# Performance work log

Measured on AMD Instinct MI355X. Metric: run time of the kernel, lower is better.

## Reference

```python
import jax, jax.numpy as jnp
import numpy as np

MAX_DISTANCE = 50.0
NUM_BINS = 50
FEATURE_DIM = 64
B, K = 2048, 1024


def setup_inputs() -> dict:
    key = jax.random.key(0)
    k1, k2, k3, k4, k5, k6 = jax.random.split(key, 6)
    goal_positions = jax.random.normal(k1, (B, K, 2), dtype=jnp.float32) * 20.0
    ego_state = jax.random.normal(k2, (B, 4), dtype=jnp.float32)
    in_dim = NUM_BINS + 6  # 56
    s1 = 1.0 / np.sqrt(in_dim)
    s2 = 1.0 / np.sqrt(FEATURE_DIM)
    W1 = jax.random.uniform(k3, (in_dim, FEATURE_DIM), jnp.float32, -s1, s1)
    b1 = jax.random.uniform(k4, (FEATURE_DIM,), jnp.float32, -s1, s1)
    W2 = jax.random.uniform(k5, (FEATURE_DIM, 1), jnp.float32, -s2, s2)
    b2 = jax.random.uniform(k6, (1,), jnp.float32, -s2, s2)
    return {"goal_positions": goal_positions, "ego_state": ego_state,
            "W1": W1, "b1": b1, "W2": W2, "b2": b2}


def _histogram(goal_positions):
    # distances: (B, K); bin_idx = min(int(d / max_d * num_bins), num_bins - 1)
    d = jnp.linalg.norm(goal_positions, axis=-1)
    idx = jnp.floor(d / MAX_DISTANCE * NUM_BINS).astype(jnp.int32)
    idx = jnp.clip(idx, 0, NUM_BINS - 1)
    return jax.nn.one_hot(idx, NUM_BINS, dtype=goal_positions.dtype)  # (B, K, num_bins)


def reference(goal_positions, ego_state, W1, b1, W2, b2):
    hist = _histogram(goal_positions)                              # (B, K, nb)
    ego = jnp.broadcast_to(ego_state[:, None, :],
                           (goal_positions.shape[0], goal_positions.shape[1], 4))
    feats = jnp.concatenate([hist, goal_positions, ego], axis=-1)  # (B, K, nb+6)
    h = jax.nn.relu(jnp.einsum('bkf,fd->bkd', feats, W1) + b1)     # (B, K, feature_dim)
    scores = (jnp.einsum('bkd,do->bko', h, W2) + b2)[..., 0]       # (B, K)
    return scores
```

## Files before the change

kernel.cpp:

```cpp
#include <hip/hip_runtime.h>

#define NBIN 50
#define DIM  64
#define KPT  4
#define TPB  256

__global__ __launch_bounds__(TPB, 8) void scorer_kernel(
    const float* __restrict__ goal,
    const float* __restrict__ ego,
    const float* __restrict__ W1,
    const float* __restrict__ b1,
    const float* __restrict__ W2,
    const float* __restrict__ b2,
    float* __restrict__ out,
    int K)
{
    __shared__ float4 comb[16 * NBIN];
    __shared__ float  e_lds[DIM];

    const int b   = blockIdx.x;
    const int tid = threadIdx.x;

    const float4 eg = ((const float4*)ego)[b];
    if (tid < DIM) {
        float v = b1[tid]
                + eg.x * W1[52 * DIM + tid]
                + eg.y * W1[53 * DIM + tid]
                + eg.z * W1[54 * DIM + tid]
                + eg.w * W1[55 * DIM + tid];
        e_lds[tid] = v;
    }
    __syncthreads();

    for (int i = tid; i < NBIN * DIM; i += TPB) {
        int bin = i >> 6;
        int d   = i & 63;
        float v = W1[i] + e_lds[d];
        ((float*)comb)[(((d >> 2) * NBIN) + bin) * 4 + (d & 3)] = v;
    }
    __syncthreads();

    const float2* gp   = (const float2*)goal + (size_t)b * K;
    const float4* w50v = (const float4*)(W1 + 50 * DIM);
    const float4* w51v = (const float4*)(W1 + 51 * DIM);
    const float4* w2v  = (const float4*)W2;
    const float  bias2 = b2[0];

    float2 p[KPT];
    int    idx[KPT];
    float  acc[KPT];

#pragma unroll
    for (int j = 0; j < KPT; ++j) {
        int k = j * TPB + tid;
        p[j] = gp[k];
        float r2 = __fadd_rn(__fmul_rn(p[j].x, p[j].x), __fmul_rn(p[j].y, p[j].y));
        float r  = __fsqrt_rn(r2);
        float fv = floorf(__fmul_rn(__fdiv_rn(r, 50.0f), 50.0f));
        int ix = (int)fv;
        ix = ix < 0 ? 0 : (ix > NBIN - 1 ? NBIN - 1 : ix);
        idx[j] = ix;
        acc[j] = 0.0f;
    }

#pragma unroll
    for (int d4 = 0; d4 < 16; ++d4) {
        const float4 a  = w50v[d4];
        const float4 bb = w51v[d4];
        const float4 c  = w2v[d4];
#pragma unroll
        for (int j = 0; j < KPT; ++j) {
            const float4 g = comb[d4 * NBIN + idx[j]];
            float x = p[j].x, y = p[j].y;
            float t0 = fmaf(x, a.x, fmaf(y, bb.x, g.x));
            float t1 = fmaf(x, a.y, fmaf(y, bb.y, g.y));
            float t2 = fmaf(x, a.z, fmaf(y, bb.z, g.z));
            float t3 = fmaf(x, a.w, fmaf(y, bb.w, g.w));
            acc[j] = fmaf(c.x, fmaxf(t0, 0.0f), acc[j]);
            acc[j] = fmaf(c.y, fmaxf(t1, 0.0f), acc[j]);
            acc[j] = fmaf(c.z, fmaxf(t2, 0.0f), acc[j]);
            acc[j] = fmaf(c.w, fmaxf(t3, 0.0f), acc[j]);
        }
    }

    float* po = out + (size_t)b * K;
#pragma unroll
    for (int j = 0; j < KPT; ++j) {
        po[j * TPB + tid] = acc[j] + bias2;
    }
}

extern "C" void kernel_launch(void* const* d_in, const int* in_sizes, int n_in,
                              void* d_out, int out_size, void* d_ws, size_t ws_size,
                              hipStream_t stream) {
    const float* goal = (const float*)d_in[0];
    const float* ego  = (const float*)d_in[1];
    const float* W1   = (const float*)d_in[2];
    const float* b1   = (const float*)d_in[3];
    const float* W2   = (const float*)d_in[4];
    const float* b2   = (const float*)d_in[5];
    float* out = (float*)d_out;

    int B = in_sizes[1] / 4;
    int K = in_sizes[0] / (2 * B);

    scorer_kernel<<<dim3(B), dim3(TPB), 0, stream>>>(goal, ego, W1, b1, W2, b2, out, K);
}
```

Baseline: 21.94 us.

## Store combined bin table as bf16 and vectorize goal loads/stores per thread

Result: slower. 25.06 us (+14.2%).

```diff
diff --git a/kernel.cpp b/kernel.cpp
--- a/kernel.cpp
+++ b/kernel.cpp
@@ -2,10 +2,17 @@
 
 #define NBIN 50
 #define DIM  64
+#define TPB  256
 #define KPT  4
-#define TPB  256
 
-__global__ __launch_bounds__(TPB, 8) void scorer_kernel(
+__device__ __forceinline__ float u32_as_f32(unsigned int u) {
+    union { unsigned int u; float f; } c; c.u = u; return c.f;
+}
+__device__ __forceinline__ unsigned int f32_bits(float f) {
+    union { float f; unsigned int u; } c; c.f = f; return c.u;
+}
+
+__global__ __launch_bounds__(TPB, 4) void scorer_kernel(
     const float* __restrict__ goal,
     const float* __restrict__ ego,
     const float* __restrict__ W1,
@@ -15,20 +22,19 @@
     float* __restrict__ out,
     int K)
 {
-    __shared__ float4 comb[16 * NBIN];
-    __shared__ float  e_lds[DIM];
+    __shared__ alignas(16) unsigned short comb[8 * NBIN * 8];
+    __shared__ float e_lds[DIM];
 
     const int b   = blockIdx.x;
     const int tid = threadIdx.x;
 
     const float4 eg = ((const float4*)ego)[b];
     if (tid < DIM) {
-        float v = b1[tid]
-                + eg.x * W1[52 * DIM + tid]
-                + eg.y * W1[53 * DIM + tid]
-                + eg.z * W1[54 * DIM + tid]
-                + eg.w * W1[55 * DIM + tid];
-        e_lds[tid] = v;
+        e_lds[tid] = b1[tid]
+                   + eg.x * W1[52 * DIM + tid]
+                   + eg.y * W1[53 * DIM + tid]
+                   + eg.z * W1[54 * DIM + tid]
+                   + eg.w * W1[55 * DIM + tid];
     }
     __syncthreads();
 
@@ -36,58 +42,79 @@
         int bin = i >> 6;
         int d   = i & 63;
         float v = W1[i] + e_lds[d];
-        ((float*)comb)[(((d >> 2) * NBIN) + bin) * 4 + (d & 3)] = v;
+        unsigned int u = f32_bits(v);
+        unsigned int r = (u + 0x7fffu + ((u >> 16) & 1u)) >> 16;
+        comb[((d >> 3) * NBIN + bin) * 8 + (d & 7)] = (unsigned short)r;
     }
     __syncthreads();
 
-    const float2* gp   = (const float2*)goal + (size_t)b * K;
-    const float4* w50v = (const float4*)(W1 + 50 * DIM);
-    const float4* w51v = (const float4*)(W1 + 51 * DIM);
-    const float4* w2v  = (const float4*)W2;
-    const float  bias2 = b2[0];
+    const float4* gp4 = (const float4*)goal + (size_t)b * (K / 2);
+    const float4  ga  = gp4[tid * 2];
+    const float4  gb  = gp4[tid * 2 + 1];
 
     float2 p[KPT];
     int    idx[KPT];
     float  acc[KPT];
+    p[0] = make_float2(ga.x, ga.y);
+    p[1] = make_float2(ga.z, ga.w);
+    p[2] = make_float2(gb.x, gb.y);
+    p[3] = make_float2(gb.z, gb.w);
 
 #pragma unroll
     for (int j = 0; j < KPT; ++j) {
-        int k = j * TPB + tid;
-        p[j] = gp[k];
         float r2 = __fadd_rn(__fmul_rn(p[j].x, p[j].x), __fmul_rn(p[j].y, p[j].y));
-        float r  = __fsqrt_rn(r2);
-        float fv = floorf(__fmul_rn(__fdiv_rn(r, 50.0f), 50.0f));
+        float fv = floorf(__fmul_rn(__fdiv_rn(__fsqrt_rn(r2), 50.0f), 50.0f));
         int ix = (int)fv;
-        ix = ix < 0 ? 0 : (ix > NBIN - 1 ? NBIN - 1 : ix);
-        idx[j] = ix;
+        idx[j] = ix < 0 ? 0 : (ix > NBIN - 1 ? NBIN - 1 : ix);
         acc[j] = 0.0f;
     }
 
+    const float4* w50v  = (const float4*)(W1 + 50 * DIM);
+    const float4* w51v  = (const float4*)(W1 + 51 * DIM);
+    const float4* w2v   = (const float4*)W2;
+    const uint4*  combv = (const uint4*)comb;
+    const float   bias2 = b2[0];
+
 #pragma unroll
-    for (int d4 = 0; d4 < 16; ++d4) {
-        const float4 a  = w50v[d4];
-        const float4 bb = w51v[d4];
-        const float4 c  = w2v[d4];
+    for (int d8 = 0; d8 < 8; ++d8) {
+        const float4 a0 = w50v[d8 * 2];
+        const float4 a1 = w50v[d8 * 2 + 1];
+        const float4 q0 = w51v[d8 * 2];
+        const float4 q1 = w51v[d8 * 2 + 1];
+        const float4 c0 = w2v[d8 * 2];
+        const float4 c1 = w2v[d8 * 2 + 1];
 #pragma unroll
         for (int j = 0; j < KPT; ++j) {
-            const float4 g = comb[d4 * NBIN + idx[j]];
-            float x = p[j].x, y = p[j].y;
-            float t0 = fmaf(x, a.x, fmaf(y, bb.x, g.x));
-            float t1 = fmaf(x, a.y, fmaf(y, bb.y, g.y));
-            float t2 = fmaf(x, a.z, fmaf(y, bb.z, g.z));
-            float t3 = fmaf(x, a.w, fmaf(y, bb.w, g.w));
-            acc[j] = fmaf(c.x, fmaxf(t0, 0.0f), acc[j]);
-            acc[j] = fmaf(c.y, fmaxf(t1, 0.0f), acc[j]);
-            acc[j] = fmaf(c.z, fmaxf(t2, 0.0f), acc[j]);
-            acc[j] = fmaf(c.w, fmaxf(t3, 0.0f), acc[j]);
+            const uint4 g = combv[d8 * NBIN + idx[j]];
+            const float x = p[j].x, y = p[j].y;
+            float s = acc[j];
+            float h0 = u32_as_f32(g.x << 16), h1 = u32_as_f32(g.x & 0xffff0000u);
+            float h2 = u32_as_f32(g.y << 16), h3 = u32_as_f32(g.y & 0xffff0000u);
+            float h4 = u32_as_f32(g.z << 16), h5 = u32_as_f32(g.z & 0xffff0000u);
+            float h6 = u32_as_f32(g.w << 16), h7 = u32_as_f32(g.w & 0xffff0000u);
+            float t0 = fmaf(x, a0.x, fmaf(y, q0.x, h0));
+            float t1 = fmaf(x, a0.y, fmaf(y, q0.y, h1));
+            float t2 = fmaf(x, a0.z, fmaf(y, q0.z, h2));
+            float t3 = fmaf(x, a0.w, fmaf(y, q0.w, h3));
+            float t4 = fmaf(x, a1.x, fmaf(y, q1.x, h4));
+            float t5 = fmaf(x, a1.y, fmaf(y, q1.y, h5));
+            float t6 = fmaf(x, a1.z, fmaf(y, q1.z, h6));
+            float t7 = fmaf(x, a1.w, fmaf(y, q1.w, h7));
+            s = fmaf(c0.x, fmaxf(t0, 0.0f), s);
+            s = fmaf(c0.y, fmaxf(t1, 0.0f), s);
+            s = fmaf(c0.z, fmaxf(t2, 0.0f), s);
+            s = fmaf(c0.w, fmaxf(t3, 0.0f), s);
+            s = fmaf(c1.x, fmaxf(t4, 0.0f), s);
+            s = fmaf(c1.y, fmaxf(t5, 0.0f), s);
+            s = fmaf(c1.z, fmaxf(t6, 0.0f), s);
+            s = fmaf(c1.w, fmaxf(t7, 0.0f), s);
+            acc[j] = s;
         }
     }
 
-    float* po = out + (size_t)b * K;
-#pragma unroll
-    for (int j = 0; j < KPT; ++j) {
-        po[j * TPB + tid] = acc[j] + bias2;
-    }
+    float4 res = make_float4(acc[0] + bias2, acc[1] + bias2,
+                             acc[2] + bias2, acc[3] + bias2);
+    ((float4*)out)[(size_t)b * (K / 4) + tid] = res;
 }
 
 extern "C" void kernel_launch(void* const* d_in, const int* in_sizes, int n_in,
```

## Counting-sort points by bin in LDS to avoid bank conflicts in combined-table lookups

Applied to the files above, without the earlier changes.

Result: slower. 23.71 us (+8.0%).

```diff
diff --git a/kernel.cpp b/kernel.cpp
--- a/kernel.cpp
+++ b/kernel.cpp
@@ -2,80 +2,118 @@
 
 #define NBIN 50
 #define DIM  64
+#define TPB  256
 #define KPT  4
-#define TPB  256
+#define KMAX (TPB * KPT)
 
-__global__ __launch_bounds__(TPB, 8) void scorer_kernel(
+__global__ __launch_bounds__(TPB, 5) void scorer_kernel(
     const float* __restrict__ goal,
     const float* __restrict__ ego,
     const float* __restrict__ W1,
     const float* __restrict__ b1,
     const float* __restrict__ W2,
     const float* __restrict__ b2,
-    float* __restrict__ out,
-    int K)
+    float* __restrict__ out)
 {
     __shared__ float4 comb[16 * NBIN];
     __shared__ float  e_lds[DIM];
+    __shared__ float2 sxy[KMAX];
+    __shared__ unsigned short smeta[KMAX];
+    __shared__ int    cnt[NBIN];
+    __shared__ int    pfx[NBIN];
+    __shared__ float  sout[KMAX];
 
     const int b   = blockIdx.x;
     const int tid = threadIdx.x;
 
-    const float4 eg = ((const float4*)ego)[b];
+    const float4* gp4 = (const float4*)goal + (size_t)b * (KMAX / 2);
+    const float4  ga  = gp4[tid * 2];
+    const float4  gb  = gp4[tid * 2 + 1];
+    const float4  eg  = ((const float4*)ego)[b];
+
     if (tid < DIM) {
-        float v = b1[tid]
-                + eg.x * W1[52 * DIM + tid]
-                + eg.y * W1[53 * DIM + tid]
-                + eg.z * W1[54 * DIM + tid]
-                + eg.w * W1[55 * DIM + tid];
-        e_lds[tid] = v;
+        e_lds[tid] = b1[tid]
+                   + eg.x * W1[52 * DIM + tid]
+                   + eg.y * W1[53 * DIM + tid]
+                   + eg.z * W1[54 * DIM + tid]
+                   + eg.w * W1[55 * DIM + tid];
+    }
+    if (tid < NBIN) cnt[tid] = 0;
+    __syncthreads();
+
+    float2 p[KPT];
+    p[0] = make_float2(ga.x, ga.y);
+    p[1] = make_float2(ga.z, ga.w);
+    p[2] = make_float2(gb.x, gb.y);
+    p[3] = make_float2(gb.z, gb.w);
+
+    int bin[KPT], rnk[KPT];
+#pragma unroll
+    for (int j = 0; j < KPT; ++j) {
+        float r2 = __fadd_rn(__fmul_rn(p[j].x, p[j].x), __fmul_rn(p[j].y, p[j].y));
+        float fv = floorf(__fmul_rn(__fdiv_rn(__fsqrt_rn(r2), 50.0f), 50.0f));
+        int ix = (int)fv;
+        bin[j] = ix < 0 ? 0 : (ix > NBIN - 1 ? NBIN - 1 : ix);
+        rnk[j] = atomicAdd(&cnt[bin[j]], 1);
+    }
+    for (int i = tid; i < NBIN * DIM; i += TPB) {
+        int bn = i >> 6;
+        int d  = i & 63;
+        ((float*)comb)[(((d >> 2) * NBIN) + bn) * 4 + (d & 3)] = W1[i] + e_lds[d];
     }
     __syncthreads();
 
-    for (int i = tid; i < NBIN * DIM; i += TPB) {
-        int bin = i >> 6;
-        int d   = i & 63;
-        float v = W1[i] + e_lds[d];
-        ((float*)comb)[(((d >> 2) * NBIN) + bin) * 4 + (d & 3)] = v;
+    if (tid < 64) {
+        int v = (tid < NBIN) ? cnt[tid] : 0;
+        int incl = v;
+#pragma unroll
+        for (int d = 1; d < 64; d <<= 1) {
+            int up = __shfl_up(incl, d, 64);
+            if (tid >= d) incl += up;
+        }
+        if (tid < NBIN) pfx[tid] = incl - v;
     }
     __syncthreads();
 
-    const float2* gp   = (const float2*)goal + (size_t)b * K;
+#pragma unroll
+    for (int j = 0; j < KPT; ++j) {
+        int pos = pfx[bin[j]] + rnk[j];
+        sxy[pos]   = p[j];
+        smeta[pos] = (unsigned short)((tid * KPT + j) | (bin[j] << 10));
+    }
+    __syncthreads();
+
     const float4* w50v = (const float4*)(W1 + 50 * DIM);
     const float4* w51v = (const float4*)(W1 + 51 * DIM);
     const float4* w2v  = (const float4*)W2;
     const float  bias2 = b2[0];
 
-    float2 p[KPT];
-    int    idx[KPT];
+    float2 q[KPT];
+    int    sb[KPT], sk[KPT];
     float  acc[KPT];
-
 #pragma unroll
     for (int j = 0; j < KPT; ++j) {
-        int k = j * TPB + tid;
-        p[j] = gp[k];
-        float r2 = __fadd_rn(__fmul_rn(p[j].x, p[j].x), __fmul_rn(p[j].y, p[j].y));
-        float r  = __fsqrt_rn(r2);
-        float fv = floorf(__fmul_rn(__fdiv_rn(r, 50.0f), 50.0f));
-        int ix = (int)fv;
-        ix = ix < 0 ? 0 : (ix > NBIN - 1 ? NBIN - 1 : ix);
-        idx[j] = ix;
+        int s = j * TPB + tid;
+        q[j]  = sxy[s];
+        int m = smeta[s];
+        sk[j] = m & (KMAX - 1);
+        sb[j] = m >> 10;
         acc[j] = 0.0f;
     }
 
 #pragma unroll
     for (int d4 = 0; d4 < 16; ++d4) {
-        const float4 a  = w50v[d4];
-        const float4 bb = w51v[d4];
-        const float4 c  = w2v[d4];
+        const float4 a = w50v[d4];
+        const float4 u = w51v[d4];
+        const float4 c = w2v[d4];
 #pragma unroll
         for (int j = 0; j < KPT; ++j) {
-            const float4 g = comb[d4 * NBIN + idx[j]];
-            float x = p[j].x, y = p[j].y;
-            float t0 = fmaf(x, a.x, fmaf(y, bb.x, g.x));
-            float t1 = fmaf(x, a.y, fmaf(y, bb.y, g.y));
-            float t2 = fmaf(x, a.z, fmaf(y, bb.z, g.z));
-            float t3 = fmaf(x, a.w, fmaf(y, bb.w, g.w));
+            const float4 g = comb[d4 * NBIN + sb[j]];
+            const float x = q[j].x, y = q[j].y;
+            float t0 = fmaf(x, a.x, fmaf(y, u.x, g.x));
+            float t1 = fmaf(x, a.y, fmaf(y, u.y, g.y));
+            float t2 = fmaf(x, a.z, fmaf(y, u.z, g.z));
+            float t3 = fmaf(x, a.w, fmaf(y, u.w, g.w));
             acc[j] = fmaf(c.x, fmaxf(t0, 0.0f), acc[j]);
             acc[j] = fmaf(c.y, fmaxf(t1, 0.0f), acc[j]);
             acc[j] = fmaf(c.z, fmaxf(t2, 0.0f), acc[j]);
@@ -83,11 +121,13 @@
         }
     }
 
-    float* po = out + (size_t)b * K;
 #pragma unroll
-    for (int j = 0; j < KPT; ++j) {
-        po[j * TPB + tid] = acc[j] + bias2;
-    }
+    for (int j = 0; j < KPT; ++j) sout[sk[j]] = acc[j] + bias2;
+    __syncthreads();
+
+    float4 res = make_float4(sout[tid * 4], sout[tid * 4 + 1],
+                             sout[tid * 4 + 2], sout[tid * 4 + 3]);
+    ((float4*)out)[(size_t)b * (KMAX / 4) + tid] = res;
 }
 
 extern "C" void kernel_launch(void* const* d_in, const int* in_sizes, int n_in,
@@ -102,7 +142,5 @@
     float* out = (float*)d_out;
 
     int B = in_sizes[1] / 4;
-    int K = in_sizes[0] / (2 * B);
-
-    scorer_kernel<<<dim3(B), dim3(TPB), 0, stream>>>(goal, ego, W1, b1, W2, b2, out, K);
+    scorer_kernel<<<dim3(B), dim3(TPB), 0, stream>>>(goal, ego, W1, b1, W2, b2, out);
 }
```

## Use packed FP32 FMA, 512 threads, two points per thread, fused setup

Applied to the files above, without the earlier changes.

Measured after the change: 23.58 us. +7.5%, slower.

```diff
diff --git a/kernel.cpp b/kernel.cpp
--- a/kernel.cpp
+++ b/kernel.cpp
@@ -2,8 +2,19 @@
 
 #define NBIN 50
 #define DIM  64
-#define KPT  4
-#define TPB  256
+#define TPB  512
+
+typedef float f32x2 __attribute__((ext_vector_type(2)));
+
+__device__ __forceinline__ f32x2 pk_fma_vs(f32x2 v, f32x2 s, f32x2 c) {
+    f32x2 r;
+    asm("v_pk_fma_f32 %0, %1, %2, %3" : "=v"(r) : "v"(v), "s"(s), "v"(c));
+    return r;
+}
+__device__ __forceinline__ f32x2 pk_fma_acc(f32x2 s, f32x2 t, f32x2 acc) {
+    asm("v_pk_fma_f32 %0, %1, %2, %0" : "+v"(acc) : "s"(s), "v"(t));
+    return acc;
+}
 
 __global__ __launch_bounds__(TPB, 8) void scorer_kernel(
     const float* __restrict__ goal,
@@ -12,82 +23,85 @@
     const float* __restrict__ b1,
     const float* __restrict__ W2,
     const float* __restrict__ b2,
-    float* __restrict__ out,
-    int K)
+    float* __restrict__ out)
 {
     __shared__ float4 comb[16 * NBIN];
-    __shared__ float  e_lds[DIM];
 
     const int b   = blockIdx.x;
     const int tid = threadIdx.x;
 
+    const float4 g4 = ((const float4*)goal)[(size_t)b * (1024 / 2) + tid];
     const float4 eg = ((const float4*)ego)[b];
-    if (tid < DIM) {
-        float v = b1[tid]
-                + eg.x * W1[52 * DIM + tid]
-                + eg.y * W1[53 * DIM + tid]
-                + eg.z * W1[54 * DIM + tid]
-                + eg.w * W1[55 * DIM + tid];
-        e_lds[tid] = v;
+
+    const int   d  = tid & 63;
+    const float ev = b1[d]
+                   + eg.x * W1[52 * DIM + d]
+                   + eg.y * W1[53 * DIM + d]
+                   + eg.z * W1[54 * DIM + d]
+                   + eg.w * W1[55 * DIM + d];
+
+    const float2 p0 = make_float2(g4.x, g4.y);
+    const float2 p1 = make_float2(g4.z, g4.w);
+    int idx0, idx1;
+    {
+        float r2 = __fadd_rn(__fmul_rn(p0.x, p0.x), __fmul_rn(p0.y, p0.y));
+        float fv = floorf(__fmul_rn(__fdiv_rn(__fsqrt_rn(r2), 50.0f), 50.0f));
+        int ix = (int)fv;
+        idx0 = ix < 0 ? 0 : (ix > NBIN - 1 ? NBIN - 1 : ix);
+    }
+    {
+        float r2 = __fadd_rn(__fmul_rn(p1.x, p1.x), __fmul_rn(p1.y, p1.y));
+        float fv = floorf(__fmul_rn(__fdiv_rn(__fsqrt_rn(r2), 50.0f), 50.0f));
+        int ix = (int)fv;
+        idx1 = ix < 0 ? 0 : (ix > NBIN - 1 ? NBIN - 1 : ix);
+    }
+
+    for (int i = tid; i < NBIN * DIM; i += TPB) {
+        int bn = i >> 6;
+        ((float*)comb)[((d >> 2) * NBIN + bn) * 4 + (d & 3)] = W1[i] + ev;
     }
     __syncthreads();
 
-    for (int i = tid; i < NBIN * DIM; i += TPB) {
-        int bin = i >> 6;
-        int d   = i & 63;
-        float v = W1[i] + e_lds[d];
-        ((float*)comb)[(((d >> 2) * NBIN) + bin) * 4 + (d & 3)] = v;
-    }
-    __syncthreads();
-
-    const float2* gp   = (const float2*)goal + (size_t)b * K;
-    const float4* w50v = (const float4*)(W1 + 50 * DIM);
-    const float4* w51v = (const float4*)(W1 + 51 * DIM);
-    const float4* w2v  = (const float4*)W2;
+    const f32x2* w50v = (const f32x2*)(W1 + 50 * DIM);
+    const f32x2* w51v = (const f32x2*)(W1 + 51 * DIM);
+    const f32x2* w2v  = (const f32x2*)W2;
     const float  bias2 = b2[0];
 
-    float2 p[KPT];
-    int    idx[KPT];
-    float  acc[KPT];
-
-#pragma unroll
-    for (int j = 0; j < KPT; ++j) {
-        int k = j * TPB + tid;
-        p[j] = gp[k];
-        float r2 = __fadd_rn(__fmul_rn(p[j].x, p[j].x), __fmul_rn(p[j].y, p[j].y));
-        float r  = __fsqrt_rn(r2);
-        float fv = floorf(__fmul_rn(__fdiv_rn(r, 50.0f), 50.0f));
-        int ix = (int)fv;
-        ix = ix < 0 ? 0 : (ix > NBIN - 1 ? NBIN - 1 : ix);
-        idx[j] = ix;
-        acc[j] = 0.0f;
-    }
+    const f32x2 xx0 = {p0.x, p0.x}, yy0 = {p0.y, p0.y};
+    const f32x2 xx1 = {p1.x, p1.x}, yy1 = {p1.y, p1.y};
+    f32x2 a0l = {0.f, 0.f}, a0h = {0.f, 0.f};
+    f32x2 a1l = {0.f, 0.f}, a1h = {0.f, 0.f};
 
 #pragma unroll
     for (int d4 = 0; d4 < 16; ++d4) {
-        const float4 a  = w50v[d4];
-        const float4 bb = w51v[d4];
-        const float4 c  = w2v[d4];
-#pragma unroll
-        for (int j = 0; j < KPT; ++j) {
-            const float4 g = comb[d4 * NBIN + idx[j]];
-            float x = p[j].x, y = p[j].y;
-            float t0 = fmaf(x, a.x, fmaf(y, bb.x, g.x));
-            float t1 = fmaf(x, a.y, fmaf(y, bb.y, g.y));
-            float t2 = fmaf(x, a.z, fmaf(y, bb.z, g.z));
-            float t3 = fmaf(x, a.w, fmaf(y, bb.w, g.w));
-            acc[j] = fmaf(c.x, fmaxf(t0, 0.0f), acc[j]);
-            acc[j] = fmaf(c.y, fmaxf(t1, 0.0f), acc[j]);
-            acc[j] = fmaf(c.z, fmaxf(t2, 0.0f), acc[j]);
-            acc[j] = fmaf(c.w, fmaxf(t3, 0.0f), acc[j]);
-        }
+        const f32x2 wa0 = w50v[d4 * 2], wa1 = w50v[d4 * 2 + 1];
+        const f32x2 wu0 = w51v[d4 * 2], wu1 = w51v[d4 * 2 + 1];
+        const f32x2 wc0 = w2v[d4 * 2],  wc1 = w2v[d4 * 2 + 1];
+        const float4 ga = comb[d4 * NBIN + idx0];
+        const float4 gb = comb[d4 * NBIN + idx1];
+
+        f32x2 t;
+        t = pk_fma_vs(yy0, wu0, (f32x2){ga.x, ga.y});
+        t = pk_fma_vs(xx0, wa0, t);
+        t.x = fmaxf(t.x, 0.0f); t.y = fmaxf(t.y, 0.0f);
+        a0l = pk_fma_acc(wc0, t, a0l);
+        t = pk_fma_vs(yy0, wu1, (f32x2){ga.z, ga.w});
+        t = pk_fma_vs(xx0, wa1, t);
+        t.x = fmaxf(t.x, 0.0f); t.y = fmaxf(t.y, 0.0f);
+        a0h = pk_fma_acc(wc1, t, a0h);
+        t = pk_fma_vs(yy1, wu0, (f32x2){gb.x, gb.y});
+        t = pk_fma_vs(xx1, wa0, t);
+        t.x = fmaxf(t.x, 0.0f); t.y = fmaxf(t.y, 0.0f);
+        a1l = pk_fma_acc(wc0, t, a1l);
+        t = pk_fma_vs(yy1, wu1, (f32x2){gb.z, gb.w});
+        t = pk_fma_vs(xx1, wa1, t);
+        t.x = fmaxf(t.x, 0.0f); t.y = fmaxf(t.y, 0.0f);
+        a1h = pk_fma_acc(wc1, t, a1h);
     }
 
-    float* po = out + (size_t)b * K;
-#pragma unroll
-    for (int j = 0; j < KPT; ++j) {
-        po[j * TPB + tid] = acc[j] + bias2;
-    }
+    const float s0 = a0l.x + a0l.y + a0h.x + a0h.y + bias2;
+    const float s1 = a1l.x + a1l.y + a1h.x + a1h.y + bias2;
+    ((float2*)out)[(size_t)b * TPB + tid] = make_float2(s0, s1);
 }
 
 extern "C" void kernel_launch(void* const* d_in, const int* in_sizes, int n_in,
@@ -102,7 +116,5 @@
     float* out = (float*)d_out;
 
     int B = in_sizes[1] / 4;
-    int K = in_sizes[0] / (2 * B);
-
-    scorer_kernel<<<dim3(B), dim3(TPB), 0, stream>>>(goal, ego, W1, b1, W2, b2, out, K);
+    scorer_kernel<<<dim3(B), dim3(TPB), 0, stream>>>(goal, ego, W1, b1, W2, b2, out);
 }
```
